# Performance work log

Hardware: AMD Instinct MI355X
Metric: run time of the kernel (lower is better)

Reference implementation:

```python
import jax, jax.numpy as jnp
import numpy as np
import math

B, S, MEM, D, H = 2, 2048, 512, 1024, 16
DH = D // H  # 64


def setup_inputs() -> dict:
    key = jax.random.key(0)
    ks = jax.random.split(key, 12)
    s = 1.0 / math.sqrt(D)
    return {
        "x": jax.random.normal(ks[0], (B, S, D), jnp.float32),
        "mems": jax.random.normal(ks[1], (B, MEM, D), jnp.float32),
        "freqs_cis": jax.random.normal(ks[2], (S, 32), jnp.float32),
        "mask": jax.random.randint(ks[3], (B, MEM + S), 0, 2, jnp.int32),
        "Wq": jax.random.normal(ks[4], (D, D), jnp.float32) * s,
        "bq": jnp.zeros((D,), jnp.float32),
        "Wk": jax.random.normal(ks[5], (D, D), jnp.float32) * s,
        "bk": jnp.zeros((D,), jnp.float32),
        "Wv": jax.random.normal(ks[6], (D, D), jnp.float32) * s,
        "bv": jnp.zeros((D,), jnp.float32),
        "Wo": jax.random.normal(ks[7], (D, D), jnp.float32) * s,
        "bo": jnp.zeros((D,), jnp.float32),
    }


def _split_heads(t):
    # [B, T, D] -> [B, H, T, DH]
    b, t_, _ = t.shape
    return t.reshape(b, t_, H, DH).transpose(0, 2, 1, 3)


def reference(x, mems, freqs_cis, mask, Wq, bq, Wk, bk, Wv, bv, Wo, bo):
    # mems prepended along sequence for K/V (torch: c = cat([mems, x], 1))
    c = jnp.concatenate([mems, x], axis=1)  # [B, MEM+S, D]
    Q = _split_heads(x @ Wq.T + bq)          # [B, H, S, DH]
    K = _split_heads(c @ Wk.T + bk)          # [B, H, Skv, DH]
    V = _split_heads(c @ Wv.T + bv)          # [B, H, Skv, DH]

    scores = jnp.einsum("bhqd,bhkd->bhqk", Q, K) / math.sqrt(DH)
    m = mask.astype(jnp.float32)             # [B, Skv]
    scores = scores - 1e6 * (1.0 - m[:, None, None, :])
    attn = jax.nn.softmax(scores, axis=-1)   # dropout omitted (eval mode)
    out = jnp.einsum("bhqk,bhkd->bhqd", attn, V)  # [B, H, S, DH]
    out = out.transpose(0, 2, 1, 3).reshape(B, S, D)
    return out @ Wo.T + bo
```

## Files before the change

### kernel.cpp

```cpp
#include <hip/hip_runtime.h>
#include <math.h>

#define NB   2
#define SQ   2048
#define SMEM 512
#define SKVN 2560
#define ND   1024
#define NH   16
#define DHN  64

typedef unsigned short u16;
typedef short bf16x8 __attribute__((ext_vector_type(8)));
typedef float f32x4 __attribute__((ext_vector_type(4)));
typedef u16 u16x4 __attribute__((ext_vector_type(4)));
typedef u16 u16x8 __attribute__((ext_vector_type(8)));

#define CSC   0.1803368801111204f

__device__ __forceinline__ u16 f2bf(float f) {
    unsigned u = __float_as_uint(f);
    u += 0x7FFFu + ((u >> 16) & 1u);
    return (u16)(u >> 16);
}

__device__ __forceinline__ void async16(u16* lds, const u16* g) {
    __builtin_amdgcn_global_load_lds(
        (const __attribute__((address_space(1))) void*)g,
        (__attribute__((address_space(3))) void*)lds, 16, 0, 0);
}

__device__ __forceinline__ unsigned lds_off(const void* p) {
    return (unsigned)(uintptr_t)(const __attribute__((address_space(3))) void*)p;
}

__device__ __forceinline__ u16x4 tr_read(unsigned a) {
    u16x4 d;
    asm volatile("ds_read_b64_tr_b16 %0, %1" : "=v"(d) : "v"(a) : "memory");
    return d;
}

__device__ __forceinline__ unsigned cvtpk(float lo, float hi) {
    unsigned r;
    asm("v_cvt_pk_bf16_f32 %0, %1, %2" : "=v"(r) : "v"(lo), "v"(hi));
    return r;
}

union PKU { unsigned u[2]; u16x4 v; };
union U8  { struct { u16x4 lo, hi; } p; bf16x8 v; };

__global__ __launch_bounds__(256)
void cvt_all(const float* __restrict__ x, const float* __restrict__ mems,
             const float* __restrict__ W0, const float* __restrict__ W1,
             const float* __restrict__ W2, const float* __restrict__ W3,
             u16* __restrict__ xb, u16* __restrict__ memb,
             u16* __restrict__ d0, u16* __restrict__ d1,
             u16* __restrict__ d2, u16* __restrict__ d3,
             const int* __restrict__ mask, float* __restrict__ mbias)
{
    const int bid = blockIdx.x;
    if (bid >= 4608) {
        const int i = (bid - 4608) * 256 + threadIdx.x;
        if (i < NB * SKVN) mbias[i] = mask[i] ? 0.f : 1.0e6f * CSC;
        return;
    }
    size_t i = ((size_t)bid * 256 + threadIdx.x) * 8;
    const float* s; u16* d;
    if (i < 4194304) { s = x; d = xb; }
    else if (i < 5242880) { s = mems; d = memb; i -= 4194304; }
    else {
        size_t off = i - 5242880;
        const int wi = (int)(off >> 20);
        i = off & 1048575;
        switch (wi) {
            case 0:  s = W0; d = d0; break;
            case 1:  s = W1; d = d1; break;
            case 2:  s = W2; d = d2; break;
            default: s = W3; d = d3; break;
        }
    }
    float4 a = *(const float4*)(s + i);
    float4 b = *(const float4*)(s + i + 4);
    u16x8 o;
    o[0]=f2bf(a.x); o[1]=f2bf(a.y); o[2]=f2bf(a.z); o[3]=f2bf(a.w);
    o[4]=f2bf(b.x); o[5]=f2bf(b.y); o[6]=f2bf(b.z); o[7]=f2bf(b.w);
    *(u16x8*)(d + i) = o;
}

__device__ __forceinline__ const u16* arow_ptr(const u16* x, const u16* mems,
                                               int grow, int T, int memLen) {
    int b = grow >= T ? 1 : 0;
    int t = grow - b * T;
    if (memLen > 0 && t < memLen)
        return mems + ((size_t)(b * memLen + t)) * ND;
    return x + ((size_t)(b * (T - memLen) + (t - memLen))) * ND;
}

__device__ __forceinline__
void gemm_body(const u16* __restrict__ x, const u16* __restrict__ mems,
               const u16* __restrict__ W, const float* __restrict__ bias,
               void* __restrict__ out, int T, int memLen, int mode,
               int bx, int by, u16* As0, u16* As1, u16* Bs0, u16* Bs1)
{
    u16* As[2] = {As0, As1};
    u16* Bs[2] = {Bs0, Bs1};

    const int tid  = threadIdx.x;
    const int wave = tid >> 6, lane = tid & 63;
    const int lg = lane >> 4, li = lane & 15;
    const int wr = (wave >> 1) * 64, wc = (wave & 1) * 64;
    const int row0 = bx * 128, col0 = by * 128;

    const int srow = lane >> 2;
    const int sslot = lane & 3;

    f32x4 acc[4][4];
    const f32x4 zf = {0.f, 0.f, 0.f, 0.f};
#pragma unroll
    for (int m = 0; m < 4; ++m)
#pragma unroll
        for (int n = 0; n < 4; ++n) acc[m][n] = zf;

    auto stage = [&](int c, int kt) {
        const int k0 = kt * 32;
#pragma unroll
        for (int ch = wave; ch < 8; ch += 4) {
            const int r = ch * 16 + srow;
            const int gs = sslot ^ ((r ^ (r >> 2)) & 3);
            async16(&As[c][ch * 512],
                    arow_ptr(x, mems, row0 + r, T, memLen) + k0 + gs * 8);
        }
#pragma unroll
        for (int ch = wave; ch < 8; ch += 4) {
            const int r = ch * 16 + srow;
            const int gs = sslot ^ ((r ^ (r >> 2)) & 3);
            async16(&Bs[c][ch * 512],
                    W + (size_t)(col0 + r) * ND + k0 + gs * 8);
        }
    };

    stage(0, 0);
    int cur = 0;
    for (int kt = 0; kt < 32; ++kt) {
        __syncthreads();
        if (kt + 1 < 32) stage(cur ^ 1, kt + 1);

        bf16x8 af[4], bfr[4];
#pragma unroll
        for (int m = 0; m < 4; ++m) {
            const int r = wr + m * 16 + li;
            af[m] = *(const bf16x8*)&As[cur][r * 32 + ((lg ^ ((r ^ (r >> 2)) & 3)) << 3)];
        }
#pragma unroll
        for (int n = 0; n < 4; ++n) {
            const int r = wc + n * 16 + li;
            bfr[n] = *(const bf16x8*)&Bs[cur][r * 32 + ((lg ^ ((r ^ (r >> 2)) & 3)) << 3)];
        }
#pragma unroll
        for (int m = 0; m < 4; ++m)
#pragma unroll
            for (int n = 0; n < 4; ++n)
                acc[m][n] = __builtin_amdgcn_mfma_f32_16x16x32_bf16(
                                af[m], bfr[n], acc[m][n], 0, 0, 0);
        cur ^= 1;
    }

#pragma unroll
    for (int n = 0; n < 4; ++n) {
        const int col = col0 + wc + n * 16 + li;
        const float bv = bias[col];
#pragma unroll
        for (int m = 0; m < 4; ++m) {
            const int rbase = row0 + wr + m * 16 + 4 * lg;
            if (mode == 0) {
                float* o = (float*)out;
#pragma unroll
                for (int r = 0; r < 4; ++r)
                    o[(size_t)(rbase + r) * ND + col] = acc[m][n][r] + bv;
            } else if (mode == 1) {
                u16* o = (u16*)out;
                const int h = col >> 6, dh = col & 63;
#pragma unroll
                for (int r = 0; r < 4; ++r) {
                    const int grow = rbase + r;
                    const int b = grow >= T ? 1 : 0;
                    const int t = grow - b * T;
                    o[(((size_t)b * NH + h) * T + t) * DHN + dh] =
                        f2bf(acc[m][n][r] + bv);
                }
            } else {
                u16* o = (u16*)out;
                const int h = col >> 6, dh = col & 63;
                const int b = rbase >= T ? 1 : 0;
                const int t = rbase - b * T;
                u16x4 pk;
                pk[0] = f2bf(acc[m][n][0] + bv);
                pk[1] = f2bf(acc[m][n][1] + bv);
                pk[2] = f2bf(acc[m][n][2] + bv);
                pk[3] = f2bf(acc[m][n][3] + bv);
                *(u16x4*)&o[(((size_t)b * NH + h) * DHN + dh) * (size_t)T + t] = pk;
            }
        }
    }
}

__global__ __launch_bounds__(256)
void gemm_single(const u16* __restrict__ x, const u16* __restrict__ W,
                 const float* __restrict__ bias, void* __restrict__ out,
                 int T, int mode)
{
    __shared__ u16 As[2][128 * 32];
    __shared__ u16 Bs[2][128 * 32];
    gemm_body(x, nullptr, W, bias, out, T, 0, mode, blockIdx.x, blockIdx.y,
              As[0], As[1], Bs[0], Bs[1]);
}

__global__ __launch_bounds__(256)
void gemm_qkv(const u16* __restrict__ xb, const u16* __restrict__ memb,
              const u16* __restrict__ Wq, const float* __restrict__ bq, u16* Qb,
              const u16* __restrict__ Wk, const float* __restrict__ bk, u16* Kb,
              const u16* __restrict__ Wv, const float* __restrict__ bv, u16* Vtb)
{
    __shared__ u16 As[2][128 * 32];
    __shared__ u16 Bs[2][128 * 32];
    const int id = (blockIdx.x & 7) * 112 + (blockIdx.x >> 3);
    if (id < 256) {
        gemm_body(xb, nullptr, Wq, bq, Qb, SQ, 0, 1, id & 31, id >> 5,
                  As[0], As[1], Bs[0], Bs[1]);
    } else if (id < 576) {
        const int t = id - 256;
        gemm_body(xb, memb, Wk, bk, Kb, SKVN, SMEM, 1, t % 40, t / 40,
                  As[0], As[1], Bs[0], Bs[1]);
    } else {
        const int t = id - 576;
        gemm_body(xb, memb, Wv, bv, Vtb, SKVN, SMEM, 2, t % 40, t / 40,
                  As[0], As[1], Bs[0], Bs[1]);
    }
}

__global__ __launch_bounds__(256)
void attn_mfma(const u16* __restrict__ Qw, const u16* __restrict__ Kw,
               const u16* __restrict__ Vt, const float* __restrict__ mbias,
               u16* __restrict__ AO)
{
    __shared__ u16 Ks[2][64 * 64];
    __shared__ u16 Vs[2][64 * 64];
    __shared__ u16 Ps[4][1024];

    const int tid  = threadIdx.x;
    const int wave = tid >> 6, lane = tid & 63;
    const int lg = lane >> 4, li = lane & 15;

    const int wg = blockIdx.x;
    const int sw = (wg & 7) * 128 + (wg >> 3);
    const int bh = sw >> 5;
    const int q0 = (sw & 31) * 64;
    const int b = bh >> 4, h = bh & 15;

    const u16* Kg = Kw + (size_t)bh * SKVN * DHN;
    const u16* Vg = Vt + (size_t)bh * DHN * SKVN;
    const float* mrow = mbias + (size_t)b * SKVN;

    bf16x8 qa0, qa1;
    {
        const u16* Qp = Qw + ((size_t)bh * SQ + q0 + wave * 16 + li) * DHN;
        qa0 = *(const bf16x8*)(Qp + lg * 8);
        qa1 = *(const bf16x8*)(Qp + 32 + lg * 8);
    }

    U8 ou;
#pragma unroll
    for (int i = 0; i < 4; ++i) { ou.p.lo[i] = 0x3F80; ou.p.hi[i] = 0x3F80; }
    const bf16x8 onesb = ou.v;

    const int srow = lane >> 3, sslot = lane & 7;

    auto stage = [&](int c, int t) {
        const int kv0 = t * 64;
#pragma unroll
        for (int ch = wave; ch < 8; ch += 4) {
            const int r = ch * 8 + srow;
            async16(&Ks[c][ch * 512],
                    Kg + (size_t)(kv0 + r) * DHN + ((sslot ^ (r & 7)) << 3));
        }
#pragma unroll
        for (int ch = wave; ch < 8; ch += 4) {
            const int r = ch * 8 + srow;
            async16(&Vs[c][ch * 512],
                    Vg + (size_t)r * SKVN + kv0 + ((sslot ^ (r & 7)) << 3));
        }
    };

    f32x4 o[4], lacc;
    const f32x4 zf = {0.f, 0.f, 0.f, 0.f};
#pragma unroll
    for (int n = 0; n < 4; ++n) o[n] = zf;
    lacc = zf;

    u16* Pw = &Ps[wave][0];
    const unsigned pa_base = lds_off(Pw) + 256u * lg + 8u * li;

    float mbn[4];
#pragma unroll
    for (int n = 0; n < 4; ++n) mbn[n] = mrow[n * 16 + li];

    stage(0, 0);
    int cur = 0;
    for (int t = 0; t < SKVN / 64; ++t) {
        float mbc[4];
#pragma unroll
        for (int n = 0; n < 4; ++n) mbc[n] = mbn[n];

        __syncthreads();
        if (t + 1 < SKVN / 64) {
            stage(cur ^ 1, t + 1);
#pragma unroll
            for (int n = 0; n < 4; ++n)
                mbn[n] = mrow[(t + 1) * 64 + n * 16 + li];
        }

        __builtin_amdgcn_s_setprio(1);
        f32x4 s[4];
#pragma unroll
        for (int n = 0; n < 4; ++n) {
            const int r = n * 16 + li;
            bf16x8 kb0 = *(const bf16x8*)&Ks[cur][r * 64 + ((lg ^ (r & 7)) << 3)];
            bf16x8 kb1 = *(const bf16x8*)&Ks[cur][r * 64 + (((4 + lg) ^ (r & 7)) << 3)];
            f32x4 z = zf;
            z    = __builtin_amdgcn_mfma_f32_16x16x32_bf16(qa0, kb0, z, 0, 0, 0);
            s[n] = __builtin_amdgcn_mfma_f32_16x16x32_bf16(qa1, kb1, z, 0, 0, 0);
        }
        __builtin_amdgcn_s_setprio(0);

#pragma unroll
        for (int n = 0; n < 4; ++n) {
            const float p0 = exp2f(fmaf(s[n][0], CSC, -mbc[n]));
            const float p1 = exp2f(fmaf(s[n][1], CSC, -mbc[n]));
            const float p2 = exp2f(fmaf(s[n][2], CSC, -mbc[n]));
            const float p3 = exp2f(fmaf(s[n][3], CSC, -mbc[n]));
            PKU u;
            u.u[0] = cvtpk(p0, p1);
            u.u[1] = cvtpk(p2, p3);
            *(u16x4*)&Pw[(n * 16 + li) * 16 + lg * 4] = u.v;
        }

        u16x4 t00 = tr_read(pa_base);
        u16x4 t01 = tr_read(pa_base + 128);
        u16x4 t10 = tr_read(pa_base + 1024);
        u16x4 t11 = tr_read(pa_base + 1024 + 128);
        asm volatile("s_waitcnt lgkmcnt(0)" ::: "memory");
        __builtin_amdgcn_sched_barrier(0);
        U8 pa0, pa1;
        pa0.p.lo = t00; pa0.p.hi = t01;
        pa1.p.lo = t10; pa1.p.hi = t11;

        __builtin_amdgcn_s_setprio(1);
        lacc = __builtin_amdgcn_mfma_f32_16x16x32_bf16(pa0.v, onesb, lacc, 0, 0, 0);
        lacc = __builtin_amdgcn_mfma_f32_16x16x32_bf16(pa1.v, onesb, lacc, 0, 0, 0);
#pragma unroll
        for (int n = 0; n < 4; ++n) {
            const int r = n * 16 + li;
            bf16x8 vb0 = *(const bf16x8*)&Vs[cur][r * 64 + ((lg ^ (r & 7)) << 3)];
            bf16x8 vb1 = *(const bf16x8*)&Vs[cur][r * 64 + (((4 + lg) ^ (r & 7)) << 3)];
            o[n] = __builtin_amdgcn_mfma_f32_16x16x32_bf16(pa0.v, vb0, o[n], 0, 0, 0);
            o[n] = __builtin_amdgcn_mfma_f32_16x16x32_bf16(pa1.v, vb1, o[n], 0, 0, 0);
        }
        __builtin_amdgcn_s_setprio(0);
        cur ^= 1;
    }

#pragma unroll
    for (int r = 0; r < 4; ++r) {
        const float inv = 1.f / lacc[r];
        const int row = q0 + wave * 16 + 4 * lg + r;
#pragma unroll
        for (int n = 0; n < 4; ++n) {
            const int col = h * DHN + n * 16 + li;
            AO[((size_t)b * SQ + row) * ND + col] = f2bf(o[n][r] * inv);
        }
    }
}

extern "C" void kernel_launch(void* const* d_in, const int* in_sizes, int n_in,
                              void* d_out, int out_size, void* d_ws, size_t ws_size,
                              hipStream_t stream)
{
    const float* x    = (const float*)d_in[0];
    const float* mems = (const float*)d_in[1];
    const int*   mask = (const int*)d_in[3];
    const float* Wq = (const float*)d_in[4];  const float* bq = (const float*)d_in[5];
    const float* Wk = (const float*)d_in[6];  const float* bk = (const float*)d_in[7];
    const float* Wv = (const float*)d_in[8];  const float* bv = (const float*)d_in[9];
    const float* Wo = (const float*)d_in[10]; const float* bo = (const float*)d_in[11];
    float* out = (float*)d_out;

    u16* ws = (u16*)d_ws;
    u16* xb   = ws;
    u16* memb = xb   + (size_t)NB * SQ * ND;
    u16* Wqb  = memb + (size_t)NB * SMEM * ND;
    u16* Wkb  = Wqb + (size_t)ND * ND;
    u16* Wvb  = Wkb + (size_t)ND * ND;
    u16* Wob  = Wvb + (size_t)ND * ND;
    u16* Qb   = Wob + (size_t)ND * ND;
    u16* Kb   = Qb  + (size_t)NB * NH * SQ * DHN;
    u16* Vtb  = Kb  + (size_t)NB * NH * SKVN * DHN;
    u16* AOb  = Vtb + (size_t)NB * NH * SKVN * DHN;
    float* mbias = (float*)(AOb + (size_t)NB * SQ * ND);

    const dim3 blk(256);
    cvt_all<<<dim3(4628), blk, 0, stream>>>(x, mems, Wq, Wk, Wv, Wo,
                                            xb, memb, Wqb, Wkb, Wvb, Wob,
                                            mask, mbias);
    gemm_qkv<<<dim3(896), blk, 0, stream>>>(xb, memb,
                                            Wqb, bq, Qb,
                                            Wkb, bk, Kb,
                                            Wvb, bv, Vtb);
    attn_mfma<<<dim3(1024), blk, 0, stream>>>(Qb, Kb, Vtb, mbias, AOb);
    gemm_single<<<dim3(32, 8), blk, 0, stream>>>(AOb, Wob, bo, (void*)out, SQ, 0);
}
```

Measured before the change: 187.4 us.

## Process two 16-row query tiles per wave in attention to reuse K/V loads

```diff
diff --git a/kernel.cpp b/kernel.cpp
--- a/kernel.cpp
+++ b/kernel.cpp
@@ -42,6 +42,12 @@
 __device__ __forceinline__ unsigned cvtpk(float lo, float hi) {
     unsigned r;
     asm("v_cvt_pk_bf16_f32 %0, %1, %2" : "=v"(r) : "v"(lo), "v"(hi));
+    return r;
+}
+
+__device__ __forceinline__ float exp2r(float x) {
+    float r;
+    asm("v_exp_f32 %0, %1" : "=v"(r) : "v"(x));
     return r;
 }
 
@@ -244,27 +250,29 @@
 {
     __shared__ u16 Ks[2][64 * 64];
     __shared__ u16 Vs[2][64 * 64];
-    __shared__ u16 Ps[4][1024];
+    __shared__ u16 Ps[4][2048];
 
     const int tid  = threadIdx.x;
     const int wave = tid >> 6, lane = tid & 63;
     const int lg = lane >> 4, li = lane & 15;
 
     const int wg = blockIdx.x;
-    const int sw = (wg & 7) * 128 + (wg >> 3);
-    const int bh = sw >> 5;
-    const int q0 = (sw & 31) * 64;
+    const int sw = (wg & 7) * 64 + (wg >> 3);
+    const int bh = sw >> 4;
+    const int q0 = (sw & 15) * 128;
     const int b = bh >> 4, h = bh & 15;
 
     const u16* Kg = Kw + (size_t)bh * SKVN * DHN;
     const u16* Vg = Vt + (size_t)bh * DHN * SKVN;
     const float* mrow = mbias + (size_t)b * SKVN;
 
-    bf16x8 qa0, qa1;
+    bf16x8 qA0, qA1, qB0, qB1;
     {
-        const u16* Qp = Qw + ((size_t)bh * SQ + q0 + wave * 16 + li) * DHN;
-        qa0 = *(const bf16x8*)(Qp + lg * 8);
-        qa1 = *(const bf16x8*)(Qp + 32 + lg * 8);
+        const u16* Qp = Qw + ((size_t)bh * SQ + q0 + wave * 32 + li) * DHN;
+        qA0 = *(const bf16x8*)(Qp + lg * 8);
+        qA1 = *(const bf16x8*)(Qp + 32 + lg * 8);
+        qB0 = *(const bf16x8*)(Qp + 16 * DHN + lg * 8);
+        qB1 = *(const bf16x8*)(Qp + 16 * DHN + 32 + lg * 8);
     }
 
     U8 ou;
@@ -290,14 +298,15 @@
         }
     };
 
-    f32x4 o[4], lacc;
+    f32x4 oA[4], oB[4], laccA, laccB;
     const f32x4 zf = {0.f, 0.f, 0.f, 0.f};
 #pragma unroll
-    for (int n = 0; n < 4; ++n) o[n] = zf;
-    lacc = zf;
+    for (int n = 0; n < 4; ++n) { oA[n] = zf; oB[n] = zf; }
+    laccA = zf; laccB = zf;
 
     u16* Pw = &Ps[wave][0];
-    const unsigned pa_base = lds_off(Pw) + 256u * lg + 8u * li;
+    const unsigned paA = lds_off(Pw) + 256u * lg + 8u * li;
+    const unsigned paB = paA + 2048u;
 
     float mbn[4];
 #pragma unroll
@@ -319,50 +328,69 @@
         }
 
         __builtin_amdgcn_s_setprio(1);
-        f32x4 s[4];
+        f32x4 sA[4], sB[4];
 #pragma unroll
         for (int n = 0; n < 4; ++n) {
             const int r = n * 16 + li;
             bf16x8 kb0 = *(const bf16x8*)&Ks[cur][r * 64 + ((lg ^ (r & 7)) << 3)];
             bf16x8 kb1 = *(const bf16x8*)&Ks[cur][r * 64 + (((4 + lg) ^ (r & 7)) << 3)];
             f32x4 z = zf;
-            z    = __builtin_amdgcn_mfma_f32_16x16x32_bf16(qa0, kb0, z, 0, 0, 0);
-            s[n] = __builtin_amdgcn_mfma_f32_16x16x32_bf16(qa1, kb1, z, 0, 0, 0);
+            z     = __builtin_amdgcn_mfma_f32_16x16x32_bf16(qA0, kb0, z, 0, 0, 0);
+            sA[n] = __builtin_amdgcn_mfma_f32_16x16x32_bf16(qA1, kb1, z, 0, 0, 0);
+            f32x4 y = zf;
+            y     = __builtin_amdgcn_mfma_f32_16x16x32_bf16(qB0, kb0, y, 0, 0, 0);
+            sB[n] = __builtin_amdgcn_mfma_f32_16x16x32_bf16(qB1, kb1, y, 0, 0, 0);
         }
         __builtin_amdgcn_s_setprio(0);
 
 #pragma unroll
         for (int n = 0; n < 4; ++n) {
-            const float p0 = exp2f(fmaf(s[n][0], CSC, -mbc[n]));
-            const float p1 = exp2f(fmaf(s[n][1], CSC, -mbc[n]));
-            const float p2 = exp2f(fmaf(s[n][2], CSC, -mbc[n]));
-            const float p3 = exp2f(fmaf(s[n][3], CSC, -mbc[n]));
-            PKU u;
-            u.u[0] = cvtpk(p0, p1);
-            u.u[1] = cvtpk(p2, p3);
-            *(u16x4*)&Pw[(n * 16 + li) * 16 + lg * 4] = u.v;
-        }
-
-        u16x4 t00 = tr_read(pa_base);
-        u16x4 t01 = tr_read(pa_base + 128);
-        u16x4 t10 = tr_read(pa_base + 1024);
-        u16x4 t11 = tr_read(pa_base + 1024 + 128);
+            const float mb = mbc[n];
+            const int pw = (n * 16 + li) * 16 + lg * 4;
+            PKU ua;
+            ua.u[0] = cvtpk(exp2r(fmaf(sA[n][0], CSC, -mb)),
+                            exp2r(fmaf(sA[n][1], CSC, -mb)));
+            ua.u[1] = cvtpk(exp2r(fmaf(sA[n][2], CSC, -mb)),
+                            exp2r(fmaf(sA[n][3], CSC, -mb)));
+            *(u16x4*)&Pw[pw] = ua.v;
+            PKU ub;
+            ub.u[0] = cvtpk(exp2r(fmaf(sB[n][0], CSC, -mb)),
+                            exp2r(fmaf(sB[n][1], CSC, -mb)));
+            ub.u[1] = cvtpk(exp2r(fmaf(sB[n][2], CSC, -mb)),
+                            exp2r(fmaf(sB[n][3], CSC, -mb)));
+            *(u16x4*)&Pw[1024 + pw] = ub.v;
+        }
+
+        u16x4 a00 = tr_read(paA);
+        u16x4 a01 = tr_read(paA + 128);
+        u16x4 a10 = tr_read(paA + 1024);
+        u16x4 a11 = tr_read(paA + 1024 + 128);
+        u16x4 b00 = tr_read(paB);
+        u16x4 b01 = tr_read(paB + 128);
+        u16x4 b10 = tr_read(paB + 1024);
+        u16x4 b11 = tr_read(paB + 1024 + 128);
         asm volatile("s_waitcnt lgkmcnt(0)" ::: "memory");
         __builtin_amdgcn_sched_barrier(0);
-        U8 pa0, pa1;
-        pa0.p.lo = t00; pa0.p.hi = t01;
-        pa1.p.lo = t10; pa1.p.hi = t11;
+        U8 pA0, pA1, pB0, pB1;
+        pA0.p.lo = a00; pA0.p.hi = a01;
+        pA1.p.lo = a10; pA1.p.hi = a11;
+        pB0.p.lo = b00; pB0.p.hi = b01;
+        pB1.p.lo = b10; pB1.p.hi = b11;
 
         __builtin_amdgcn_s_setprio(1);
-        lacc = __builtin_amdgcn_mfma_f32_16x16x32_bf16(pa0.v, onesb, lacc, 0, 0, 0);
-        lacc = __builtin_amdgcn_mfma_f32_16x16x32_bf16(pa1.v, onesb, lacc, 0, 0, 0);
+        laccA = __builtin_amdgcn_mfma_f32_16x16x32_bf16(pA0.v, onesb, laccA, 0, 0, 0);
+        laccA = __builtin_amdgcn_mfma_f32_16x16x32_bf16(pA1.v, onesb, laccA, 0, 0, 0);
+        laccB = __builtin_amdgcn_mfma_f32_16x16x32_bf16(pB0.v, onesb, laccB, 0, 0, 0);
+        laccB = __builtin_amdgcn_mfma_f32_16x16x32_bf16(pB1.v, onesb, laccB, 0, 0, 0);
 #pragma unroll
         for (int n = 0; n < 4; ++n) {
             const int r = n * 16 + li;
             bf16x8 vb0 = *(const bf16x8*)&Vs[cur][r * 64 + ((lg ^ (r & 7)) << 3)];
             bf16x8 vb1 = *(const bf16x8*)&Vs[cur][r * 64 + (((4 + lg) ^ (r & 7)) << 3)];
-            o[n] = __builtin_amdgcn_mfma_f32_16x16x32_bf16(pa0.v, vb0, o[n], 0, 0, 0);
-            o[n] = __builtin_amdgcn_mfma_f32_16x16x32_bf16(pa1.v, vb1, o[n], 0, 0, 0);
+            oA[n] = __builtin_amdgcn_mfma_f32_16x16x32_bf16(pA0.v, vb0, oA[n], 0, 0, 0);
+            oA[n] = __builtin_amdgcn_mfma_f32_16x16x32_bf16(pA1.v, vb1, oA[n], 0, 0, 0);
+            oB[n] = __builtin_amdgcn_mfma_f32_16x16x32_bf16(pB0.v, vb0, oB[n], 0, 0, 0);
+            oB[n] = __builtin_amdgcn_mfma_f32_16x16x32_bf16(pB1.v, vb1, oB[n], 0, 0, 0);
         }
         __builtin_amdgcn_s_setprio(0);
         cur ^= 1;
@@ -370,12 +398,14 @@
 
 #pragma unroll
     for (int r = 0; r < 4; ++r) {
-        const float inv = 1.f / lacc[r];
-        const int row = q0 + wave * 16 + 4 * lg + r;
+        const float invA = 1.f / laccA[r];
+        const float invB = 1.f / laccB[r];
+        const int rowA = q0 + wave * 32 + 4 * lg + r;
 #pragma unroll
         for (int n = 0; n < 4; ++n) {
             const int col = h * DHN + n * 16 + li;
-            AO[((size_t)b * SQ + row) * ND + col] = f2bf(o[n][r] * inv);
+            AO[((size_t)b * SQ + rowA) * ND + col] = f2bf(oA[n][r] * invA);
+            AO[((size_t)b * SQ + rowA + 16) * ND + col] = f2bf(oB[n][r] * invB);
         }
     }
 }
@@ -414,6 +444,6 @@
                                             Wqb, bq, Qb,
                                             Wkb, bk, Kb,
                                             Wvb, bv, Vtb);
-    attn_mfma<<<dim3(1024), blk, 0, stream>>>(Qb, Kb, Vtb, mbias, AOb);
+    attn_mfma<<<dim3(512), blk, 0, stream>>>(Qb, Kb, Vtb, mbias, AOb);
     gemm_single<<<dim3(32, 8), blk, 0, stream>>>(AOb, Wob, bo, (void*)out, SQ, 0);
 }
```

Result: faster. 172.8 us (-7.8%).
